# Optimization experiments

Measured on AMD Instinct MI355X. Metric: run time of the kernel, lower is better.

The kernel has to match this reference:

```python
import jax, jax.numpy as jnp
import numpy as np

N_COMP = 5
EPS = 0.1
BATCH = 2_097_152
BISECT_ITERS = 60
LAM_HI = 1e6  # upper bracket for the KL-constraint Lagrange multiplier


def setup_inputs() -> dict:
    key = jax.random.key(0)
    kx, kw, kb = jax.random.split(key, 3)
    # Positive inputs/weights keep q = x @ W.T + b > 0 (cp.kl_div domain).
    x = jax.random.uniform(kx, (BATCH, N_COMP), dtype=jnp.float32)
    W = jax.random.uniform(kw, (N_COMP, N_COMP), dtype=jnp.float32) * 0.5
    b = jax.random.uniform(kb, (N_COMP,), dtype=jnp.float32) * 0.5 + 0.1
    return {"x": x, "W": W, "b": b}


def _kl_ball_project(q, eps):
    """Solve min_p sum(kl_div(p,q)) s.t. sum(kl_div(p,r)) <= eps, sum(p)=1, p>=0
    with r = uniform (the module's first-call r_prev = ones/n, sum(r)=1).

    With sum(p)=1 the extra (-p + q) / (-p + r) terms of cp.kl_div are constants,
    so this is min KL(p||q) s.t. KL(p||r) <= eps on the simplex. KKT gives the
    closed-form geometric-mixture path p(lam) ~ q^{1/(1+lam)} * r^{lam/(1+lam)};
    we bisect on lam >= 0 to hit KL(p||r) = eps (lam=0 if already feasible).
    """
    n = q.shape[-1]
    logq = jnp.log(q)                                   # [B, n]
    log_r = -jnp.log(jnp.float32(n))                    # uniform r

    def p_of(lam, lq):
        t = (1.0 / (1.0 + lam))[..., None]              # [B, 1]
        return jax.nn.softmax(t * lq + (1.0 - t) * log_r, axis=-1)

    def g(lam, lq):  # constraint residual KL(p(lam) || r) - eps, shape [B]
        p = p_of(lam, lq)
        return jnp.sum(p * (jnp.log(p) - log_r), axis=-1) - eps

    # Bisection on a stop-gradient copy: lam is treated as a constant w.r.t. q
    # (envelope-style), so no solver iterations are stored for autodiff.
    lq_sg = jax.lax.stop_gradient(logq)
    zeros = jnp.zeros(q.shape[:-1], q.dtype)
    g0 = g(zeros, lq_sg)                                # feasibility at lam=0

    def body(carry, _):
        lo, hi = carry
        mid = 0.5 * (lo + hi)
        gm = g(mid, lq_sg)
        lo = jnp.where(gm > 0, mid, lo)
        hi = jnp.where(gm > 0, hi, mid)
        return (lo, hi), None

    (lo, hi), _ = jax.lax.scan(body, (zeros, jnp.full_like(zeros, LAM_HI)),
                               None, length=BISECT_ITERS)
    lam = jnp.where(g0 <= 0, 0.0, 0.5 * (lo + hi))      # exact 0 if feasible
    return p_of(lam, logq)


def reference(x, W, b):
    q = x @ W.T + b                                     # nn.Linear
    return _kl_ball_project(q, EPS)
```

## Files before the change

### kernel.cpp

```cpp
#include <hip/hip_runtime.h>
#include <math.h>

#define NC 5
#define EPS_F 0.1f

__global__ __launch_bounds__(256) void klproj_kernel(
    const float* __restrict__ x,
    const float* __restrict__ W,
    const float* __restrict__ b,
    float* __restrict__ out,
    int batch)
{
    int row = blockIdx.x * blockDim.x + threadIdx.x;
    if (row >= batch) return;

    float xv[NC];
#pragma unroll
    for (int k = 0; k < NC; ++k) xv[k] = x[row * NC + k];

    float s[NC];
    float m = -1e30f;
#pragma unroll
    for (int j = 0; j < NC; ++j) {
        float q = b[j];
#pragma unroll
        for (int k = 0; k < NC; ++k) q = fmaf(xv[k], W[j * NC + k], q);
        float sj = __logf(q);
        s[j] = sj;
        m = fmaxf(m, sj);
    }
    float u[NC];
#pragma unroll
    for (int j = 0; j < NC; ++j) u[j] = s[j] - m;

    const float logn = 1.6094379124341003f;

    auto eval = [&](float t, float& f, float& fp) {
        float Z = 0.f, T1 = 0.f, T2 = 0.f;
#pragma unroll
        for (int j = 0; j < NC; ++j) {
            float ej = __expf(t * u[j]);
            Z += ej;
            T1 = fmaf(ej, u[j], T1);
            T2 = fmaf(ej, u[j] * u[j], T2);
        }
        float rZ = 1.0f / Z;
        float Eu = T1 * rZ;
        float Eu2 = T2 * rZ;
        f  = fmaf(t, Eu, -__logf(Z)) + (logn - EPS_F);
        fp = t * (Eu2 - Eu * Eu);
    };

    float f1, fp1;
    eval(1.0f, f1, fp1);

    float t = 1.0f;
    if (f1 > 0.f) {
        float lo = 0.f, hi = 1.0f;
        float cand = 1.0f - f1 / fp1;
        t = (cand > lo && cand < hi) ? cand : 0.5f;
#pragma unroll
        for (int it = 0; it < 8; ++it) {
            float f, fp;
            eval(t, f, fp);
            if (f > 0.f) hi = t; else lo = t;
            float tn = t - f / fp;
            t = (tn > lo && tn < hi) ? tn : 0.5f * (lo + hi);
        }
    }

    float e[NC], Z = 0.f;
#pragma unroll
    for (int j = 0; j < NC; ++j) { e[j] = __expf(t * u[j]); Z += e[j]; }
    float rZ = 1.0f / Z;
#pragma unroll
    for (int j = 0; j < NC; ++j) out[row * NC + j] = e[j] * rZ;
}

extern "C" void kernel_launch(void* const* d_in, const int* in_sizes, int n_in,
                              void* d_out, int out_size, void* d_ws, size_t ws_size,
                              hipStream_t stream) {
    const float* x = (const float*)d_in[0];
    const float* W = (const float*)d_in[1];
    const float* b = (const float*)d_in[2];
    float* out = (float*)d_out;
    int batch = in_sizes[0] / NC;

    int block = 256;
    int grid = (batch + block - 1) / block;
    klproj_kernel<<<grid, block, 0, stream>>>(x, W, b, out, batch);
}
```

Before: 94.80 us.

## Process two rows per thread with interleaved Newton iterations and cheaper initial guess

Each thread now handles two rows (i and i+half) and interleaves their safeguarded Newton iterations to raise instruction-level parallelism. It precomputes u squared, uses hardware reciprocal intrinsics instead of IEEE division, seeds t from an rsqrt-based estimate of the KL at t=1, and cuts the iterations from 8 to 6. The aim is to hide transcendental latency and reduce ALU work. The trade-offs are lower accuracy from fewer iterations and approximate reciprocals, and an odd batch size would leave the last row unprocessed.

```diff
diff --git a/kernel.cpp b/kernel.cpp
--- a/kernel.cpp
+++ b/kernel.cpp
@@ -4,77 +4,99 @@
 #define NC 5
 #define EPS_F 0.1f
 
+__device__ __forceinline__ float frcp(float v) { return __builtin_amdgcn_rcpf(v); }
+
 __global__ __launch_bounds__(256) void klproj_kernel(
     const float* __restrict__ x,
     const float* __restrict__ W,
     const float* __restrict__ b,
     float* __restrict__ out,
-    int batch)
+    int half)
 {
-    int row = blockIdx.x * blockDim.x + threadIdx.x;
-    if (row >= batch) return;
+    int i = blockIdx.x * blockDim.x + threadIdx.x;
+    if (i >= half) return;
 
-    float xv[NC];
+    const float C = 1.6094379124341003f - EPS_F;
+
+    float u[2][NC], u2[2][NC], t[2], lo[2], hi[2], f1[2];
+
 #pragma unroll
-    for (int k = 0; k < NC; ++k) xv[k] = x[row * NC + k];
+    for (int r = 0; r < 2; ++r) {
+        int row = i + r * half;
+        float xv[NC];
+#pragma unroll
+        for (int k = 0; k < NC; ++k) xv[k] = x[row * NC + k];
+        float s[NC];
+        float m = -1e30f;
+#pragma unroll
+        for (int j = 0; j < NC; ++j) {
+            float q = b[j];
+#pragma unroll
+            for (int k = 0; k < NC; ++k) q = fmaf(xv[k], W[j * NC + k], q);
+            s[j] = __logf(q);
+            m = fmaxf(m, s[j]);
+        }
+#pragma unroll
+        for (int j = 0; j < NC; ++j) {
+            u[r][j]  = s[j] - m;
+            u2[r][j] = u[r][j] * u[r][j];
+        }
+    }
 
-    float s[NC];
-    float m = -1e30f;
-#pragma unroll
-    for (int j = 0; j < NC; ++j) {
-        float q = b[j];
-#pragma unroll
-        for (int k = 0; k < NC; ++k) q = fmaf(xv[k], W[j * NC + k], q);
-        float sj = __logf(q);
-        s[j] = sj;
-        m = fmaxf(m, sj);
-    }
-    float u[NC];
-#pragma unroll
-    for (int j = 0; j < NC; ++j) u[j] = s[j] - m;
-
-    const float logn = 1.6094379124341003f;
-
-    auto eval = [&](float t, float& f, float& fp) {
+    auto eval = [&](int r, float tt, float& f, float& fp) {
         float Z = 0.f, T1 = 0.f, T2 = 0.f;
 #pragma unroll
         for (int j = 0; j < NC; ++j) {
-            float ej = __expf(t * u[j]);
+            float ej = __expf(tt * u[r][j]);
             Z += ej;
-            T1 = fmaf(ej, u[j], T1);
-            T2 = fmaf(ej, u[j] * u[j], T2);
+            T1 = fmaf(ej, u[r][j], T1);
+            T2 = fmaf(ej, u2[r][j], T2);
         }
-        float rZ = 1.0f / Z;
+        float rZ = frcp(Z);
         float Eu = T1 * rZ;
-        float Eu2 = T2 * rZ;
-        f  = fmaf(t, Eu, -__logf(Z)) + (logn - EPS_F);
-        fp = t * (Eu2 - Eu * Eu);
+        f  = fmaf(tt, Eu, C - __logf(Z));
+        fp = tt * fmaf(-Eu, Eu, T2 * rZ);
     };
 
-    float f1, fp1;
-    eval(1.0f, f1, fp1);
+    bool any = false;
+#pragma unroll
+    for (int r = 0; r < 2; ++r) {
+        float fp1;
+        eval(r, 1.0f, f1[r], fp1);
+        lo[r] = 0.f; hi[r] = 1.f;
+        float kl1 = f1[r] + EPS_F;
+        float t0  = 0.316227766017f * __frsqrt_rn(kl1);
+        t[r] = (t0 > 0.f && t0 < 1.f) ? t0 : 0.5f;
+        any = any || (f1[r] > 0.f);
+    }
 
-    float t = 1.0f;
-    if (f1 > 0.f) {
-        float lo = 0.f, hi = 1.0f;
-        float cand = 1.0f - f1 / fp1;
-        t = (cand > lo && cand < hi) ? cand : 0.5f;
+    if (any) {
 #pragma unroll
-        for (int it = 0; it < 8; ++it) {
-            float f, fp;
-            eval(t, f, fp);
-            if (f > 0.f) hi = t; else lo = t;
-            float tn = t - f / fp;
-            t = (tn > lo && tn < hi) ? tn : 0.5f * (lo + hi);
+        for (int it = 0; it < 6; ++it) {
+#pragma unroll
+            for (int r = 0; r < 2; ++r) {
+                float f, fp;
+                eval(r, t[r], f, fp);
+                bool pos = f > 0.f;
+                hi[r] = pos ? t[r] : hi[r];
+                lo[r] = pos ? lo[r] : t[r];
+                float tn = t[r] - f * frcp(fp);
+                t[r] = (tn > lo[r] && tn < hi[r]) ? tn : 0.5f * (lo[r] + hi[r]);
+            }
         }
     }
 
-    float e[NC], Z = 0.f;
 #pragma unroll
-    for (int j = 0; j < NC; ++j) { e[j] = __expf(t * u[j]); Z += e[j]; }
-    float rZ = 1.0f / Z;
+    for (int r = 0; r < 2; ++r) {
+        float tf = (f1[r] > 0.f) ? t[r] : 1.0f;
+        float e[NC], Z = 0.f;
 #pragma unroll
-    for (int j = 0; j < NC; ++j) out[row * NC + j] = e[j] * rZ;
+        for (int j = 0; j < NC; ++j) { e[j] = __expf(tf * u[r][j]); Z += e[j]; }
+        float rZ = frcp(Z);
+        int row = i + r * half;
+#pragma unroll
+        for (int j = 0; j < NC; ++j) out[row * NC + j] = e[j] * rZ;
+    }
 }
 
 extern "C" void kernel_launch(void* const* d_in, const int* in_sizes, int n_in,
@@ -85,8 +107,9 @@
     const float* b = (const float*)d_in[2];
     float* out = (float*)d_out;
     int batch = in_sizes[0] / NC;
+    int half = batch / 2;
 
     int block = 256;
-    int grid = (batch + block - 1) / block;
-    klproj_kernel<<<grid, block, 0, stream>>>(x, W, b, out, batch);
+    int grid = (half + block - 1) / block;
+    klproj_kernel<<<grid, block, 0, stream>>>(x, W, b, out, half);
 }
```

New measurement: 95.97 us, median of 2. No clear change (+1.2%).
